# Optimization experiments

Measured on AMD Instinct MI355X. Metric: run time of the kernel, lower is better.

Reference implementation:

```python
import jax, jax.numpy as jnp
import numpy as np

C_IN = 128      # in_channels == num_hiddens (required for residual add)
C_RES = 64      # num_residual_hiddens
D = 512         # representation_dim (in == out)


def _complete_conv1d(x, W, Wc, bc):
    """Faithful fused form of CompleteConv1d.forward for batch=1.

    x:  (1, C, D)   input
    W:  (C, D, D)   stacked per-channel Linear weights (W[c] maps D->D)
    Wc: (OC, C)     1x1 Conv1d weight (kernel dim squeezed)
    bc: (OC,)       1x1 Conv1d bias

    The autograd jacobian of the per-channel linear map is block diagonal:
      xy_grad[c, o, c', i] = W[c, o, i] * delta(c, c')
    so xy_grad_reduced[o, i] = sum_c W[c, o, i], node[i] = argmax_o of that,
    and the python double loop is a scatter-add:
      (y - y_neg)[0, f, n] = sum_{i : node[i]==n} W[f, n, i] * x[0, f, i]
    (y itself, including the Linear biases, cancels exactly).
    """
    d = W.shape[1]
    node = jnp.argmax(jnp.sum(W, axis=0), axis=0)          # (D,) argmax over o
    idx = jnp.arange(d)
    vals = W[:, node, idx] * x[0]                           # (C, D): W[f,node[i],i]*x[0,f,i]
    diff = jnp.zeros_like(x[0]).at[:, node].add(vals)       # scatter-add over repeated nodes
    out = jnp.einsum('oc,cd->od', Wc, diff) + bc[:, None]   # 1x1 conv == channel GEMM
    return out[None]                                        # (1, OC, D)


def setup_inputs() -> dict:
    key = jax.random.key(0)
    ks = jax.random.split(key, 7)
    s = lambda k, shape, scale: (jax.random.normal(k, shape, dtype=jnp.float32) * scale)
    return {
        'x':   s(ks[0], (1, C_IN, D), 1.0),
        'W1':  s(ks[1], (C_IN, D, D), D ** -0.5),
        'Wc1': s(ks[2], (C_RES, C_IN), C_IN ** -0.5),
        'bc1': s(ks[3], (C_RES,), 0.02),
        'W2':  s(ks[4], (C_RES, D, D), D ** -0.5),
        'Wc2': s(ks[5], (C_IN, C_RES), C_RES ** -0.5),
        'bc2': s(ks[6], (C_IN,), 0.02),
    }


def reference(x, W1, Wc1, bc1, W2, Wc2, bc2):
    # nn.ReLU(True) inside the Sequential mutates x in place, so the residual
    # add uses relu(x), not x.
    xr = jax.nn.relu(x)
    h1 = _complete_conv1d(xr, W1, Wc1, bc1)
    h2 = _complete_conv1d(jax.nn.relu(h1), W2, Wc2, bc2)
    return xr + h2
```

## Files before the change

kernel.cpp:

```cpp
#include <hip/hip_runtime.h>

#define C_IN  128
#define C_RES 64
#define D     512
#define DD    (D * D)

template <int C>
__device__ inline float4 colsum(const float4* __restrict__ Wp) {
    float4 acc = make_float4(0.f, 0.f, 0.f, 0.f);
#pragma unroll 16
    for (int c = 0; c < C; ++c) {
        float4 w = Wp[(size_t)c * (DD / 4)];
        acc.x += w.x; acc.y += w.y; acc.z += w.z; acc.w += w.w;
    }
    return acc;
}

__global__ void sum_zero_kernel(const float* __restrict__ W1,
                                const float* __restrict__ W2,
                                float* __restrict__ S1,
                                float* __restrict__ S2,
                                float* __restrict__ diff_zero) {
    int t = blockIdx.x * 256 + threadIdx.x;
    if (t < DD / 4) {
        ((float4*)S1)[t] = colsum<C_IN>((const float4*)W1 + t);
    } else {
        int t2 = t - DD / 4;
        ((float4*)S2)[t2] = colsum<C_RES>((const float4*)W2 + t2);
    }
    diff_zero[t] = 0.f;
}

__global__ void argmax_scatter_kernel(const float* __restrict__ S1,
                                      const float* __restrict__ S2,
                                      const float* __restrict__ W1,
                                      const float* __restrict__ W2,
                                      const float* __restrict__ x,
                                      float* __restrict__ diff1,
                                      float* __restrict__ w2v,
                                      int* __restrict__ node2) {
    __shared__ float lv[256];
    __shared__ int   li[256];
    __shared__ int   node_s[16];

    const int  tid = threadIdx.x;
    const bool st1 = blockIdx.x < 32;
    const int  i0  = (blockIdx.x & 31) * 16;
    const float* __restrict__ S = st1 ? S1 : S2;

    const int il = tid & 15;
    const int ol = tid >> 4;
    float best = -__builtin_inff();
    int   bidx = D;
#pragma unroll 4
    for (int k = 0; k < 32; ++k) {
        int o = ol + (k << 4);
        float v = S[o * D + i0 + il];
        if (v > best) { best = v; bidx = o; }
    }
    lv[tid] = best; li[tid] = bidx;
    __syncthreads();
    for (int s = 128; s >= 16; s >>= 1) {
        if (tid < s) {
            float v2 = lv[tid + s]; int i2 = li[tid + s];
            if (v2 > lv[tid] || (v2 == lv[tid] && i2 < li[tid])) {
                lv[tid] = v2; li[tid] = i2;
            }
        }
        __syncthreads();
    }
    if (tid < 16) {
        node_s[tid] = li[tid];
        if (!st1) node2[i0 + tid] = li[tid];
    }
    __syncthreads();

    if (st1) {
        for (int idx = tid; idx < C_IN * 16; idx += 256) {
            int ii = idx & 15;
            int c  = idx >> 4;
            int i  = i0 + ii;
            int n  = node_s[ii];
            float xv = fmaxf(x[c * D + i], 0.f);
            float w  = W1[(size_t)c * DD + (size_t)n * D + i];
            atomicAdd(&diff1[c * D + n], w * xv);
        }
    } else {
        for (int idx = tid; idx < C_RES * 16; idx += 256) {
            int ii = idx & 15;
            int c  = idx >> 4;
            int i  = i0 + ii;
            int n  = node_s[ii];
            w2v[c * D + i] = W2[(size_t)c * DD + (size_t)n * D + i];
        }
    }
}

__global__ void conv1_scatter2_kernel(const float* __restrict__ Wc1,
                                      const float* __restrict__ bc1,
                                      const float* __restrict__ diff1,
                                      const float* __restrict__ w2v,
                                      const int* __restrict__ node2,
                                      float* __restrict__ diff2) {
    __shared__ float wc[C_IN];
    const int c = blockIdx.x >> 1;
    const int i = ((blockIdx.x & 1) << 8) + threadIdx.x;
    if (threadIdx.x < C_IN) wc[threadIdx.x] = Wc1[c * C_IN + threadIdx.x];
    __syncthreads();

    float acc = bc1[c];
#pragma unroll 8
    for (int cc = 0; cc < C_IN; ++cc)
        acc += wc[cc] * diff1[cc * D + i];
    float x2 = fmaxf(acc, 0.f);
    int n = node2[i];
    atomicAdd(&diff2[c * D + n], w2v[c * D + i] * x2);
}

__global__ void final_kernel(const float* __restrict__ Wc2,
                             const float* __restrict__ bc2,
                             const float* __restrict__ diff2,
                             const float* __restrict__ x,
                             float* __restrict__ out) {
    __shared__ float wc[C_RES];
    const int o = blockIdx.x >> 1;
    const int d = ((blockIdx.x & 1) << 8) + threadIdx.x;
    if (threadIdx.x < C_RES) wc[threadIdx.x] = Wc2[o * C_RES + threadIdx.x];
    __syncthreads();

    float acc = bc2[o];
#pragma unroll 8
    for (int c = 0; c < C_RES; ++c)
        acc += wc[c] * diff2[c * D + d];
    out[o * D + d] = acc + fmaxf(x[o * D + d], 0.f);
}

extern "C" void kernel_launch(void* const* d_in, const int* in_sizes, int n_in,
                              void* d_out, int out_size, void* d_ws, size_t ws_size,
                              hipStream_t stream) {
    const float* x   = (const float*)d_in[0];
    const float* W1  = (const float*)d_in[1];
    const float* Wc1 = (const float*)d_in[2];
    const float* bc1 = (const float*)d_in[3];
    const float* W2  = (const float*)d_in[4];
    const float* Wc2 = (const float*)d_in[5];
    const float* bc2 = (const float*)d_in[6];
    float* out = (float*)d_out;

    float* ws    = (float*)d_ws;
    float* S1    = ws;
    float* S2    = S1 + DD;
    float* diff1 = S2 + DD;
    float* diff2 = diff1 + C_IN * D;
    float* w2v   = diff2 + C_RES * D;
    int*   node2 = (int*)(w2v + C_RES * D);

    sum_zero_kernel<<<384, 256, 0, stream>>>(W1, W2, S1, S2, diff1);
    argmax_scatter_kernel<<<64, 256, 0, stream>>>(S1, S2, W1, W2, x,
                                                  diff1, w2v, node2);
    conv1_scatter2_kernel<<<128, 256, 0, stream>>>(Wc1, bc1, diff1, w2v,
                                                   node2, diff2);
    final_kernel<<<256, 256, 0, stream>>>(Wc2, bc2, diff2, x, out);
}
```

Measured before the change: 257.0 us.

## Fuse four kernels into one cooperative kernel with grid syncs

```diff
diff --git a/kernel.cpp b/kernel.cpp
--- a/kernel.cpp
+++ b/kernel.cpp
@@ -1,138 +1,146 @@
 #include <hip/hip_runtime.h>
+#include <hip/hip_cooperative_groups.h>
+
+namespace cg = cooperative_groups;
 
 #define C_IN  128
 #define C_RES 64
 #define D     512
 #define DD    (D * D)
 
-template <int C>
-__device__ inline float4 colsum(const float4* __restrict__ Wp) {
-    float4 acc = make_float4(0.f, 0.f, 0.f, 0.f);
+#define NBLK  384
+#define NTHR  256
+
+__global__ void __launch_bounds__(NTHR, 2)
+fused_kernel(const float* __restrict__ W1,  const float* __restrict__ W2,
+             const float* __restrict__ Wc1, const float* __restrict__ bc1,
+             const float* __restrict__ Wc2, const float* __restrict__ bc2,
+             const float* __restrict__ x,
+             float* __restrict__ S1,   float* __restrict__ S2,
+             float* __restrict__ diff1,
+             float* __restrict__ w2v,  int* __restrict__ node2,
+             float* __restrict__ out) {
+    cg::grid_group grid = cg::this_grid();
+    const int tid  = threadIdx.x;
+    const int bid  = blockIdx.x;
+    const int gtid = bid * NTHR + tid;
+
+    float* __restrict__ diff2 = diff1 + C_IN * D;
+
+    if (gtid < DD / 4) {
+        const float4* Wp = (const float4*)W1 + gtid;
+        float4 acc = make_float4(0.f, 0.f, 0.f, 0.f);
 #pragma unroll 16
-    for (int c = 0; c < C; ++c) {
-        float4 w = Wp[(size_t)c * (DD / 4)];
-        acc.x += w.x; acc.y += w.y; acc.z += w.z; acc.w += w.w;
+        for (int c = 0; c < C_IN; ++c) {
+            float4 w = Wp[(size_t)c * (DD / 4)];
+            acc.x += w.x; acc.y += w.y; acc.z += w.z; acc.w += w.w;
+        }
+        ((float4*)S1)[gtid] = acc;
+    } else {
+        int t2 = gtid - DD / 4;
+        const float4* Wp = (const float4*)W2 + t2;
+        float4 acc = make_float4(0.f, 0.f, 0.f, 0.f);
+#pragma unroll 16
+        for (int c = 0; c < C_RES; ++c) {
+            float4 w = Wp[(size_t)c * (DD / 4)];
+            acc.x += w.x; acc.y += w.y; acc.z += w.z; acc.w += w.w;
+        }
+        ((float4*)S2)[t2] = acc;
     }
-    return acc;
-}
+    diff1[gtid] = 0.f;
 
-__global__ void sum_zero_kernel(const float* __restrict__ W1,
-                                const float* __restrict__ W2,
-                                float* __restrict__ S1,
-                                float* __restrict__ S2,
-                                float* __restrict__ diff_zero) {
-    int t = blockIdx.x * 256 + threadIdx.x;
-    if (t < DD / 4) {
-        ((float4*)S1)[t] = colsum<C_IN>((const float4*)W1 + t);
-    } else {
-        int t2 = t - DD / 4;
-        ((float4*)S2)[t2] = colsum<C_RES>((const float4*)W2 + t2);
-    }
-    diff_zero[t] = 0.f;
-}
+    grid.sync();
 
-__global__ void argmax_scatter_kernel(const float* __restrict__ S1,
-                                      const float* __restrict__ S2,
-                                      const float* __restrict__ W1,
-                                      const float* __restrict__ W2,
-                                      const float* __restrict__ x,
-                                      float* __restrict__ diff1,
-                                      float* __restrict__ w2v,
-                                      int* __restrict__ node2) {
-    __shared__ float lv[256];
-    __shared__ int   li[256];
-    __shared__ int   node_s[16];
+    if (bid < 64) {
+        __shared__ float lv[NTHR];
+        __shared__ int   li[NTHR];
+        __shared__ int   node_s[16];
 
-    const int  tid = threadIdx.x;
-    const bool st1 = blockIdx.x < 32;
-    const int  i0  = (blockIdx.x & 31) * 16;
-    const float* __restrict__ S = st1 ? S1 : S2;
+        const bool st1 = bid < 32;
+        const int  i0  = (bid & 31) * 16;
+        const float* __restrict__ S = st1 ? S1 : S2;
 
-    const int il = tid & 15;
-    const int ol = tid >> 4;
-    float best = -__builtin_inff();
-    int   bidx = D;
+        const int il = tid & 15;
+        const int ol = tid >> 4;
+        float best = -__builtin_inff();
+        int   bidx = D;
 #pragma unroll 4
-    for (int k = 0; k < 32; ++k) {
-        int o = ol + (k << 4);
-        float v = S[o * D + i0 + il];
-        if (v > best) { best = v; bidx = o; }
-    }
-    lv[tid] = best; li[tid] = bidx;
-    __syncthreads();
-    for (int s = 128; s >= 16; s >>= 1) {
-        if (tid < s) {
-            float v2 = lv[tid + s]; int i2 = li[tid + s];
-            if (v2 > lv[tid] || (v2 == lv[tid] && i2 < li[tid])) {
-                lv[tid] = v2; li[tid] = i2;
+        for (int k = 0; k < 32; ++k) {
+            int o = ol + (k << 4);
+            float v = S[o * D + i0 + il];
+            if (v > best) { best = v; bidx = o; }
+        }
+        lv[tid] = best; li[tid] = bidx;
+        __syncthreads();
+        for (int s = 128; s >= 16; s >>= 1) {
+            if (tid < s) {
+                float v2 = lv[tid + s]; int i2 = li[tid + s];
+                if (v2 > lv[tid] || (v2 == lv[tid] && i2 < li[tid])) {
+                    lv[tid] = v2; li[tid] = i2;
+                }
+            }
+            __syncthreads();
+        }
+        if (tid < 16) {
+            node_s[tid] = li[tid];
+            if (!st1) node2[i0 + tid] = li[tid];
+        }
+        __syncthreads();
+
+        if (st1) {
+            for (int idx = tid; idx < C_IN * 16; idx += NTHR) {
+                int ii = idx & 15;
+                int c  = idx >> 4;
+                int i  = i0 + ii;
+                int n  = node_s[ii];
+                float xv = fmaxf(x[c * D + i], 0.f);
+                float w  = W1[(size_t)c * DD + (size_t)n * D + i];
+                atomicAdd(&diff1[c * D + n], w * xv);
+            }
+        } else {
+            for (int idx = tid; idx < C_RES * 16; idx += NTHR) {
+                int ii = idx & 15;
+                int c  = idx >> 4;
+                int i  = i0 + ii;
+                int n  = node_s[ii];
+                w2v[c * D + i] = W2[(size_t)c * DD + (size_t)n * D + i];
             }
         }
+    }
+
+    grid.sync();
+
+    if (bid < 128) {
+        __shared__ float wc[C_IN];
+        const int c = bid >> 1;
+        const int i = ((bid & 1) << 8) + tid;
+        if (tid < C_IN) wc[tid] = Wc1[c * C_IN + tid];
         __syncthreads();
+
+        float acc = bc1[c];
+#pragma unroll 8
+        for (int cc = 0; cc < C_IN; ++cc)
+            acc += wc[cc] * diff1[cc * D + i];
+        float x2 = fmaxf(acc, 0.f);
+        int n = node2[i];
+        atomicAdd(&diff2[c * D + n], w2v[c * D + i] * x2);
     }
-    if (tid < 16) {
-        node_s[tid] = li[tid];
-        if (!st1) node2[i0 + tid] = li[tid];
+
+    grid.sync();
+
+    if (bid < 256) {
+        __shared__ float wc[C_RES];
+        const int o = bid >> 1;
+        const int d = ((bid & 1) << 8) + tid;
+        if (tid < C_RES) wc[tid] = Wc2[o * C_RES + tid];
+        __syncthreads();
+
+        float acc = bc2[o];
+#pragma unroll 8
+        for (int c = 0; c < C_RES; ++c)
+            acc += wc[c] * diff2[c * D + d];
+        out[o * D + d] = acc + fmaxf(x[o * D + d], 0.f);
     }
-    __syncthreads();
-
-    if (st1) {
-        for (int idx = tid; idx < C_IN * 16; idx += 256) {
-            int ii = idx & 15;
-            int c  = idx >> 4;
-            int i  = i0 + ii;
-            int n  = node_s[ii];
-            float xv = fmaxf(x[c * D + i], 0.f);
-            float w  = W1[(size_t)c * DD + (size_t)n * D + i];
-            atomicAdd(&diff1[c * D + n], w * xv);
-        }
-    } else {
-        for (int idx = tid; idx < C_RES * 16; idx += 256) {
-            int ii = idx & 15;
-            int c  = idx >> 4;
-            int i  = i0 + ii;
-            int n  = node_s[ii];
-            w2v[c * D + i] = W2[(size_t)c * DD + (size_t)n * D + i];
-        }
-    }
-}
-
-__global__ void conv1_scatter2_kernel(const float* __restrict__ Wc1,
-                                      const float* __restrict__ bc1,
-                                      const float* __restrict__ diff1,
-                                      const float* __restrict__ w2v,
-                                      const int* __restrict__ node2,
-                                      float* __restrict__ diff2) {
-    __shared__ float wc[C_IN];
-    const int c = blockIdx.x >> 1;
-    const int i = ((blockIdx.x & 1) << 8) + threadIdx.x;
-    if (threadIdx.x < C_IN) wc[threadIdx.x] = Wc1[c * C_IN + threadIdx.x];
-    __syncthreads();
-
-    float acc = bc1[c];
-#pragma unroll 8
-    for (int cc = 0; cc < C_IN; ++cc)
-        acc += wc[cc] * diff1[cc * D + i];
-    float x2 = fmaxf(acc, 0.f);
-    int n = node2[i];
-    atomicAdd(&diff2[c * D + n], w2v[c * D + i] * x2);
-}
-
-__global__ void final_kernel(const float* __restrict__ Wc2,
-                             const float* __restrict__ bc2,
-                             const float* __restrict__ diff2,
-                             const float* __restrict__ x,
-                             float* __restrict__ out) {
-    __shared__ float wc[C_RES];
-    const int o = blockIdx.x >> 1;
-    const int d = ((blockIdx.x & 1) << 8) + threadIdx.x;
-    if (threadIdx.x < C_RES) wc[threadIdx.x] = Wc2[o * C_RES + threadIdx.x];
-    __syncthreads();
-
-    float acc = bc2[o];
-#pragma unroll 8
-    for (int c = 0; c < C_RES; ++c)
-        acc += wc[c] * diff2[c * D + d];
-    out[o * D + d] = acc + fmaxf(x[o * D + d], 0.f);
 }
 
 extern "C" void kernel_launch(void* const* d_in, const int* in_sizes, int n_in,
@@ -151,14 +159,14 @@
     float* S1    = ws;
     float* S2    = S1 + DD;
     float* diff1 = S2 + DD;
-    float* diff2 = diff1 + C_IN * D;
-    float* w2v   = diff2 + C_RES * D;
+    float* w2v   = diff1 + (C_IN + C_RES) * D;
     int*   node2 = (int*)(w2v + C_RES * D);
 
-    sum_zero_kernel<<<384, 256, 0, stream>>>(W1, W2, S1, S2, diff1);
-    argmax_scatter_kernel<<<64, 256, 0, stream>>>(S1, S2, W1, W2, x,
-                                                  diff1, w2v, node2);
-    conv1_scatter2_kernel<<<128, 256, 0, stream>>>(Wc1, bc1, diff1, w2v,
-                                                   node2, diff2);
-    final_kernel<<<256, 256, 0, stream>>>(Wc2, bc2, diff2, x, out);
+    void* args[] = {
+        (void*)&W1, (void*)&W2, (void*)&Wc1, (void*)&bc1, (void*)&Wc2,
+        (void*)&bc2, (void*)&x, (void*)&S1, (void*)&S2, (void*)&diff1,
+        (void*)&w2v, (void*)&node2, (void*)&out,
+    };
+    hipLaunchCooperativeKernel((void*)fused_kernel, dim3(NBLK), dim3(NTHR),
+                               args, 0, stream);
 }
```

New measurement: 390.7 us. 1.52x slower.

## Split channel reduction into four partial sums across more blocks, widen argmax grid

Applied to the files above, without the earlier changes.

```diff
diff --git a/kernel.cpp b/kernel.cpp
--- a/kernel.cpp
+++ b/kernel.cpp
@@ -4,35 +4,53 @@
 #define C_RES 64
 #define D     512
 #define DD    (D * D)
+#define U4    (DD / 4)
 
-template <int C>
-__device__ inline float4 colsum(const float4* __restrict__ Wp) {
-    float4 acc = make_float4(0.f, 0.f, 0.f, 0.f);
-#pragma unroll 16
-    for (int c = 0; c < C; ++c) {
-        float4 w = Wp[(size_t)c * (DD / 4)];
-        acc.x += w.x; acc.y += w.y; acc.z += w.z; acc.w += w.w;
-    }
-    return acc;
+__device__ inline void acc4(float4& a, const float4& w) {
+    a.x += w.x; a.y += w.y; a.z += w.z; a.w += w.w;
 }
 
-__global__ void sum_zero_kernel(const float* __restrict__ W1,
-                                const float* __restrict__ W2,
-                                float* __restrict__ S1,
-                                float* __restrict__ S2,
-                                float* __restrict__ diff_zero) {
-    int t = blockIdx.x * 256 + threadIdx.x;
-    if (t < DD / 4) {
-        ((float4*)S1)[t] = colsum<C_IN>((const float4*)W1 + t);
-    } else {
-        int t2 = t - DD / 4;
-        ((float4*)S2)[t2] = colsum<C_RES>((const float4*)W2 + t2);
-    }
-    diff_zero[t] = 0.f;
+__device__ inline void sum8(float4& a, const float4* __restrict__ p, int stride) {
+    float4 r0 = p[0 * (size_t)stride];
+    float4 r1 = p[1 * (size_t)stride];
+    float4 r2 = p[2 * (size_t)stride];
+    float4 r3 = p[3 * (size_t)stride];
+    float4 r4 = p[4 * (size_t)stride];
+    float4 r5 = p[5 * (size_t)stride];
+    float4 r6 = p[6 * (size_t)stride];
+    float4 r7 = p[7 * (size_t)stride];
+    acc4(a, r0); acc4(a, r1); acc4(a, r2); acc4(a, r3);
+    acc4(a, r4); acc4(a, r5); acc4(a, r6); acc4(a, r7);
 }
 
-__global__ void argmax_scatter_kernel(const float* __restrict__ S1,
-                                      const float* __restrict__ S2,
+__global__ void __launch_bounds__(256, 4)
+sum_kernel(const float* __restrict__ W1, const float* __restrict__ W2,
+           float* __restrict__ P1, float* __restrict__ P2,
+           float* __restrict__ diff_zero) {
+    const int gtid = blockIdx.x * 256 + threadIdx.x;
+    const int u = gtid & (U4 - 1);
+    const int p = gtid >> 16;
+
+    const float4* w1p = (const float4*)W1 + (size_t)(32 * p) * U4 + u;
+    float4 a1 = make_float4(0.f, 0.f, 0.f, 0.f);
+    sum8(a1, w1p + (size_t)0  * U4, U4);
+    sum8(a1, w1p + (size_t)8  * U4, U4);
+    sum8(a1, w1p + (size_t)16 * U4, U4);
+    sum8(a1, w1p + (size_t)24 * U4, U4);
+    ((float4*)P1)[p * U4 + u] = a1;
+
+    const float4* w2p = (const float4*)W2 + (size_t)(16 * p) * U4 + u;
+    float4 a2 = make_float4(0.f, 0.f, 0.f, 0.f);
+    sum8(a2, w2p + (size_t)0 * U4, U4);
+    sum8(a2, w2p + (size_t)8 * U4, U4);
+    ((float4*)P2)[p * U4 + u] = a2;
+
+    if (gtid < (C_IN + C_RES) * D)
+        diff_zero[gtid] = 0.f;
+}
+
+__global__ void argmax_scatter_kernel(const float* __restrict__ P1,
+                                      const float* __restrict__ P2,
                                       const float* __restrict__ W1,
                                       const float* __restrict__ W2,
                                       const float* __restrict__ x,
@@ -41,26 +59,27 @@
                                       int* __restrict__ node2) {
     __shared__ float lv[256];
     __shared__ int   li[256];
-    __shared__ int   node_s[16];
+    __shared__ int   node_s[8];
 
     const int  tid = threadIdx.x;
-    const bool st1 = blockIdx.x < 32;
-    const int  i0  = (blockIdx.x & 31) * 16;
-    const float* __restrict__ S = st1 ? S1 : S2;
+    const int  bid = blockIdx.x;
+    const bool st1 = bid < 64;
+    const int  i0  = (st1 ? bid : bid - 64) * 8;
+    const float* __restrict__ P = st1 ? P1 : P2;
 
-    const int il = tid & 15;
-    const int ol = tid >> 4;
+    const int il = tid & 7;
+    const int ol = tid >> 3;
     float best = -__builtin_inff();
     int   bidx = D;
-#pragma unroll 4
-    for (int k = 0; k < 32; ++k) {
-        int o = ol + (k << 4);
-        float v = S[o * D + i0 + il];
+    for (int k = 0; k < 16; ++k) {
+        int o = ol + (k << 5);
+        int base = o * D + i0 + il;
+        float v = P[base] + P[DD + base] + P[2 * DD + base] + P[3 * DD + base];
         if (v > best) { best = v; bidx = o; }
     }
     lv[tid] = best; li[tid] = bidx;
     __syncthreads();
-    for (int s = 128; s >= 16; s >>= 1) {
+    for (int s = 128; s >= 8; s >>= 1) {
         if (tid < s) {
             float v2 = lv[tid + s]; int i2 = li[tid + s];
             if (v2 > lv[tid] || (v2 == lv[tid] && i2 < li[tid])) {
@@ -69,16 +88,16 @@
         }
         __syncthreads();
     }
-    if (tid < 16) {
+    if (tid < 8) {
         node_s[tid] = li[tid];
         if (!st1) node2[i0 + tid] = li[tid];
     }
     __syncthreads();
 
     if (st1) {
-        for (int idx = tid; idx < C_IN * 16; idx += 256) {
-            int ii = idx & 15;
-            int c  = idx >> 4;
+        for (int idx = tid; idx < C_IN * 8; idx += 256) {
+            int ii = idx & 7;
+            int c  = idx >> 3;
             int i  = i0 + ii;
             int n  = node_s[ii];
             float xv = fmaxf(x[c * D + i], 0.f);
@@ -86,9 +105,9 @@
             atomicAdd(&diff1[c * D + n], w * xv);
         }
     } else {
-        for (int idx = tid; idx < C_RES * 16; idx += 256) {
-            int ii = idx & 15;
-            int c  = idx >> 4;
+        for (int idx = tid; idx < C_RES * 8; idx += 256) {
+            int ii = idx & 7;
+            int c  = idx >> 3;
             int i  = i0 + ii;
             int n  = node_s[ii];
             w2v[c * D + i] = W2[(size_t)c * DD + (size_t)n * D + i];
@@ -148,16 +167,16 @@
     float* out = (float*)d_out;
 
     float* ws    = (float*)d_ws;
-    float* S1    = ws;
-    float* S2    = S1 + DD;
-    float* diff1 = S2 + DD;
+    float* P1    = ws;
+    float* P2    = P1 + 4 * DD;
+    float* diff1 = P2 + 4 * DD;
     float* diff2 = diff1 + C_IN * D;
     float* w2v   = diff2 + C_RES * D;
     int*   node2 = (int*)(w2v + C_RES * D);
 
-    sum_zero_kernel<<<384, 256, 0, stream>>>(W1, W2, S1, S2, diff1);
-    argmax_scatter_kernel<<<64, 256, 0, stream>>>(S1, S2, W1, W2, x,
-                                                  diff1, w2v, node2);
+    sum_kernel<<<1024, 256, 0, stream>>>(W1, W2, P1, P2, diff1);
+    argmax_scatter_kernel<<<128, 256, 0, stream>>>(P1, P2, W1, W2, x,
+                                                   diff1, w2v, node2);
     conv1_scatter2_kernel<<<128, 256, 0, stream>>>(Wc1, bc1, diff1, w2v,
                                                    node2, diff2);
     final_kernel<<<256, 256, 0, stream>>>(Wc2, bc2, diff2, x, out);
```

Result: slower. 269.2 us (+4.8%).
